# Optimization experiments

Hardware: AMD Instinct MI355X
Metric: run time of the kernel (lower is better)

The kernel has to match this reference:

```python
import jax, jax.numpy as jnp
import numpy as np
import math

V, D, L, FF, H, DH, W, DM, T, B = 32000, 1024, 4, 4096, 16, 64, 256, 64, 1024, 1


def rms_norm(x, w):
    return x * jax.lax.rsqrt(jnp.mean(x * x, axis=-1, keepdims=True) + 1e-6) * w


def setup_inputs() -> dict:
    key = jax.random.key(0)
    ks = jax.random.split(key, 16)
    s = 0.02
    return {
        "x": jax.random.randint(ks[0], (B, T), 0, V),
        "embed": jax.random.normal(ks[1], (V, D), jnp.float32) * s,
        "ln_in_w": jnp.ones((D,), jnp.float32),
        "ln1_w": jnp.ones((L, D), jnp.float32),
        "lnd_w": jnp.ones((L, D), jnp.float32),
        "qkv_w": jax.random.normal(ks[2], (L, 3 * H * DH, D), jnp.float32) * s,
        "swa_out_w": jax.random.normal(ks[3], (L, D, H * DH), jnp.float32) * s,
        "k_w": jax.random.normal(ks[4], (L, H * DM, D), jnp.float32) * s,
        "v_w": jax.random.normal(ks[5], (L, H * DM, D), jnp.float32) * s,
        "q_w": jax.random.normal(ks[6], (L, H * DM, D), jnp.float32) * s,
        "beta_w": jax.random.normal(ks[7], (L, H, D), jnp.float32) * s,
        "mem_out_w": jax.random.normal(ks[8], (L, D, H * DM), jnp.float32) * s,
        "gate_w": jax.random.normal(ks[9], (L, D, D), jnp.float32) * s,
        "comb_w": jax.random.normal(ks[10], (L, D, D), jnp.float32) * s,
        "ln2_w": jnp.ones((L, D), jnp.float32),
        "wg": jax.random.normal(ks[11], (L, FF, D), jnp.float32) * s,
        "wu": jax.random.normal(ks[12], (L, FF, D), jnp.float32) * s,
        "wo": jax.random.normal(ks[13], (L, D, FF), jnp.float32) * s,
        "ln_out_w": jnp.ones((D,), jnp.float32),
    }


def _swa(h1, qkv_w, out_w):
    # h1: [B,T,D]
    qkv = jnp.einsum('btd,ed->bte', h1, qkv_w)  # [B,T,3*H*DH]
    q, k, v = jnp.split(qkv, 3, axis=-1)
    q = q.reshape(h1.shape[0], T, H, DH).transpose(0, 2, 1, 3)
    k = k.reshape(h1.shape[0], T, H, DH).transpose(0, 2, 1, 3)
    v = v.reshape(h1.shape[0], T, H, DH).transpose(0, 2, 1, 3)
    scores = jnp.einsum('bhqd,bhkd->bhqk', q, k) * (DH ** -0.5)
    pos = jnp.arange(T)
    dist = pos[:, None] - pos[None, :]
    allowed = (dist >= 0) & (dist < W)  # causal sliding window
    scores = jnp.where(allowed[None, None], scores, -jnp.inf)
    attn = jax.nn.softmax(scores, axis=-1)
    out = jnp.einsum('bhqk,bhkd->bhqd', attn, v)
    out = out.transpose(0, 2, 1, 3).reshape(h1.shape[0], T, H * DH)
    return jnp.einsum('bte,de->btd', out, out_w)


def _delta(h2, k_w, v_w, q_w, beta_w, mem_out_w):
    Bv = h2.shape[0]
    proj = lambda w: jnp.einsum('btd,ed->bte', h2, w).reshape(Bv, T, H, DM).transpose(0, 2, 1, 3)
    keys, values, queries = proj(k_w), proj(v_w), proj(q_w)
    beta = jax.nn.sigmoid(jnp.einsum('btd,hd->bht', h2, beta_w))  # [B,H,T]
    keys = keys / jnp.maximum(jnp.linalg.norm(keys, axis=-1, keepdims=True), 1e-12)
    queries = queries / jnp.maximum(jnp.linalg.norm(queries, axis=-1, keepdims=True), 1e-12)
    log_retain = jnp.log(1.0 - beta + 1e-8)
    cum_log = jnp.cumsum(log_retain, axis=-1)  # [B,H,T]
    log_decay = cum_log[..., :, None] - cum_log[..., None, :]  # [B,H,T,T]
    causal = jnp.triu(jnp.ones((T, T), dtype=bool))  # matches torch.triu mask in source
    decay = jnp.exp(jnp.minimum(log_decay, 0.0)) * causal
    kq = jnp.einsum('bhid,bhjd->bhij', queries, keys) / math.sqrt(DM)
    weights = kq * decay
    out = jnp.einsum('bhij,bhjd->bhid', weights, values)
    out = out + beta[..., None] * values
    out = out.transpose(0, 2, 1, 3).reshape(Bv, T, H * DM)
    return jnp.einsum('bte,de->btd', out, mem_out_w)


def reference(x, embed, ln_in_w, ln1_w, lnd_w, qkv_w, swa_out_w, k_w, v_w, q_w,
              beta_w, mem_out_w, gate_w, comb_w, ln2_w, wg, wu, wo, ln_out_w):
    h = rms_norm(embed[x], ln_in_w)  # [B,T,D]
    for l in range(L):
        h1 = rms_norm(h, ln1_w[l])
        h2 = rms_norm(h, lnd_w[l])
        local = _swa(h1, qkv_w[l], swa_out_w[l])
        global_ctx = _delta(h2, k_w[l], v_w[l], q_w[l], beta_w[l], mem_out_w[l])
        gate = jax.nn.sigmoid(jnp.einsum('btd,ed->bte', h1, gate_w[l]))
        mixed = jnp.einsum('btd,ed->bte', gate * local + (1.0 - gate) * global_ctx, comb_w[l])
        h = h + mixed
        hn = rms_norm(h, ln2_w[l])
        ffn = jnp.einsum('btf,df->btd', jax.nn.silu(jnp.einsum('btd,fd->btf', hn, wg[l])) * jnp.einsum('btd,fd->btf', hn, wu[l]), wo[l])
        h = h + ffn
    logits = jnp.einsum('btd,vd->btv', rms_norm(h, ln_out_w), embed)  # tied head
    return logits
```

## Files before the change

kernel.cpp:

```cpp
#include <hip/hip_runtime.h>

typedef unsigned short u16;
typedef unsigned int   u32;
typedef __attribute__((ext_vector_type(8))) __bf16 bfv8;
typedef __attribute__((ext_vector_type(4))) float  f32x4;
typedef __attribute__((ext_vector_type(4))) u32    u32x4;

__device__ __forceinline__ u16 f2bf(float f){
  u32 u = __builtin_bit_cast(u32, f);
  return (u16)((u + 0x7FFFu + ((u >> 16) & 1u)) >> 16);
}
__device__ __forceinline__ float bf2f(u16 b){
  return __builtin_bit_cast(float, ((u32)b) << 16);
}
__device__ __forceinline__ u32 pk2(float a, float b){
  return (u32)f2bf(a) | ((u32)f2bf(b) << 16);
}
__device__ __forceinline__ float wsum(float v){
  #pragma unroll
  for (int m = 32; m > 0; m >>= 1) v += __shfl_xor(v, m, 64);
  return v;
}
__device__ __forceinline__ void gload16(const void* g, void* l){
  __builtin_amdgcn_global_load_lds((const __attribute__((address_space(1))) void*)g,
                                   (__attribute__((address_space(3))) void*)l, 16, 0, 0);
}

struct CBatch { const float* s[12]; long long p4[13]; u16* dst; };
__global__ __launch_bounds__(256) void flm_conv(CBatch cb)
{
  const int seg = blockIdx.y;
  const long long base = cb.p4[seg];
  const long long n8 = (cb.p4[seg + 1] - base) >> 1;
  const f32x4* __restrict__ src = (const f32x4*)cb.s[seg];
  u32x4* __restrict__ dst = (u32x4*)cb.dst + (base >> 1);
  for (long long i = (long long)blockIdx.x * 256 + threadIdx.x; i < n8;
       i += (long long)gridDim.x * 256){
    f32x4 v0 = __builtin_nontemporal_load(src + 2*i);
    f32x4 v1 = __builtin_nontemporal_load(src + 2*i + 1);
    u32x4 p;
    p.x = pk2(v0.x, v0.y); p.y = pk2(v0.z, v0.w);
    p.z = pk2(v1.x, v1.y); p.w = pk2(v1.z, v1.w);
    __builtin_nontemporal_store(p, dst + i);
  }
}

struct GDesc {
  const u16* A; const float* Bw; float* Cf; u16* Cb;
  int lda, ldb, ldc, kbeg, kend, blk0, epi, pad;
};
struct GBatch { GDesc d[6]; int ng, total; };

template<bool BW>
__global__ __launch_bounds__(512) void flm_mgemm(GBatch gb)
{
  constexpr int LDK = BW ? 64 : 72;
  __shared__ u16 sA[128][LDK];
  __shared__ u16 sB[128][LDK];
  const int tid = threadIdx.x, lane = tid & 63, w = tid >> 6;

  const int T = gb.total, bid = blockIdx.x;
  const int q8 = T >> 3, r8 = T & 7, xc = bid & 7, of = bid >> 3;
  const int lin = (xc < r8 ? xc * (q8 + 1) : r8 * (q8 + 1) + (xc - r8) * q8) + of;
  int di = 0;
  #pragma unroll
  for (int i = 1; i < 6; i++) if (i < gb.ng && lin >= gb.d[i].blk0) di = i;
  const GDesc g = gb.d[di];
  const int local = lin - g.blk0;
  const int row0 = (local & 7) * 128;
  const int col0 = (local >> 3) * 128;
  const int wr = (w >> 2) * 64, wc = (w & 3) * 32;

  f32x4 acc[4][2];
  #pragma unroll
  for (int m = 0; m < 4; m++)
    #pragma unroll
    for (int n = 0; n < 2; n++)
      acc[m][n] = (f32x4){0.f, 0.f, 0.f, 0.f};

  const int csw = ((lane & 7) ^ (lane >> 3)) * 8;
  const u16* B16 = (const u16*)g.Bw;

  for (int k0 = g.kbeg; k0 < g.kend; k0 += 64){
    if constexpr (BW){
      const u16* a0 = g.A + (size_t)(row0 + w*16 + (lane>>3)) * g.lda + k0 + csw;
      const u16* b0 = B16 + (size_t)(col0 + w*16 + (lane>>3)) * g.ldb + k0 + csw;
      gload16(a0,                     &sA[w*16    ][0]);
      gload16(a0 + (size_t)8*g.lda,   &sA[w*16 + 8][0]);
      gload16(b0,                     &sB[w*16    ][0]);
      gload16(b0 + (size_t)8*g.ldb,   &sB[w*16 + 8][0]);
    } else {
      #pragma unroll
      for (int i = 0; i < 2; i++){
        int idx = tid + i * 512;
        int r = idx >> 3, c = (idx & 7) * 8;
        *(uint4*)&sA[r][c] = *(const uint4*)(g.A + (size_t)(row0 + r) * g.lda + k0 + c);
      }
      #pragma unroll
      for (int i = 0; i < 4; i++){
        int idx = tid + i * 512;
        int r = idx >> 4, c = (idx & 15) * 4;
        float4 v = *(const float4*)(g.Bw + (size_t)(col0 + r) * g.ldb + k0 + c);
        uint2 p; p.x = pk2(v.x, v.y); p.y = pk2(v.z, v.w);
        *(uint2*)&sB[r][c] = p;
      }
    }
    __syncthreads();
    #pragma unroll
    for (int kk = 0; kk < 2; kk++){
      bfv8 af[4], bfr[2];
      #pragma unroll
      for (int m = 0; m < 4; m++){
        int row = wr + m*16 + (lane & 15);
        if constexpr (BW){
          int slot = (kk*4 + (lane >> 4)) ^ (row & 7);
          af[m] = *(const bfv8*)((const char*)sA + row*128 + slot*16);
        } else {
          af[m] = *(const bfv8*)&sA[row][kk*32 + (lane >> 4) * 8];
        }
      }
      #pragma unroll
      for (int n = 0; n < 2; n++){
        int row = wc + n*16 + (lane & 15);
        if constexpr (BW){
          int slot = (kk*4 + (lane >> 4)) ^ (row & 7);
          bfr[n] = *(const bfv8*)((const char*)sB + row*128 + slot*16);
        } else {
          bfr[n] = *(const bfv8*)&sB[row][kk*32 + (lane >> 4) * 8];
        }
      }
      #pragma unroll
      for (int m = 0; m < 4; m++)
        #pragma unroll
        for (int n = 0; n < 2; n++)
          acc[m][n] = __builtin_amdgcn_mfma_f32_16x16x32_bf16(af[m], bfr[n], acc[m][n], 0, 0, 0);
    }
    __syncthreads();
  }

  #pragma unroll
  for (int m = 0; m < 4; m++){
    int rbase = row0 + wr + m*16 + (lane >> 4) * 4;
    #pragma unroll
    for (int n = 0; n < 2; n++){
      int col = col0 + wc + n*16 + (lane & 15);
      if (g.epi == 2){
        uint2 p;
        p.x = pk2(acc[m][n][0], acc[m][n][1]);
        p.y = pk2(acc[m][n][2], acc[m][n][3]);
        *(uint2*)&g.Cb[(size_t)col * g.ldc + rbase] = p;
      } else {
        #pragma unroll
        for (int j = 0; j < 4; j++){
          float v = acc[m][n][j];
          size_t o = (size_t)(rbase + j) * g.ldc + col;
          switch (g.epi){
            case 0: g.Cf[o] = v; break;
            case 1: g.Cb[o] = f2bf(v); break;
            default: atomicAdd(&g.Cf[o], v); break;
          }
        }
      }
    }
  }
}

__global__ __launch_bounds__(256) void flm_mix(
    const float* __restrict__ gr, const float* __restrict__ lo,
    const float* __restrict__ gl, u16* __restrict__ o)
{
  int i = blockIdx.x * 256 + threadIdx.x;
  float4 gv = ((const float4*)gr)[i];
  float4 lv = ((const float4*)lo)[i];
  float4 bv = ((const float4*)gl)[i];
  float sx = 1.f/(1.f+expf(-gv.x)), sy = 1.f/(1.f+expf(-gv.y));
  float sz = 1.f/(1.f+expf(-gv.z)), sw = 1.f/(1.f+expf(-gv.w));
  uint2 p;
  p.x = pk2(sx*lv.x + (1.f-sx)*bv.x, sy*lv.y + (1.f-sy)*bv.y);
  p.y = pk2(sz*lv.z + (1.f-sz)*bv.z, sw*lv.w + (1.f-sw)*bv.w);
  ((uint2*)o)[i] = p;
}

__global__ __launch_bounds__(256) void flm_silu(
    const u16* __restrict__ gg, const u16* __restrict__ uu, u16* __restrict__ o)
{
  int i = blockIdx.x * 256 + threadIdx.x;
  uint2 gv = ((const uint2*)gg)[i];
  uint2 uv = ((const uint2*)uu)[i];
  float g0 = bf2f((u16)gv.x), g1 = bf2f((u16)(gv.x >> 16));
  float g2 = bf2f((u16)gv.y), g3 = bf2f((u16)(gv.y >> 16));
  float u0 = bf2f((u16)uv.x), u1 = bf2f((u16)(uv.x >> 16));
  float u2 = bf2f((u16)uv.y), u3 = bf2f((u16)(uv.y >> 16));
  float a = g0 / (1.f + expf(-g0)) * u0;
  float b = g1 / (1.f + expf(-g1)) * u1;
  float c = g2 / (1.f + expf(-g2)) * u2;
  float d = g3 / (1.f + expf(-g3)) * u3;
  uint2 p; p.x = pk2(a, b); p.y = pk2(c, d);
  ((uint2*)o)[i] = p;
}

__global__ __launch_bounds__(256) void flm_embed(
    const int* __restrict__ x, const float* __restrict__ embed,
    const float* __restrict__ w, float* __restrict__ h)
{
  int t = blockIdx.x, tid = threadIdx.x;
  int tok = x[t];
  float4 v = ((const float4*)(embed + (size_t)tok * 1024))[tid];
  float ss = v.x*v.x + v.y*v.y + v.z*v.z + v.w*v.w;
  ss = wsum(ss);
  __shared__ float red[4];
  if ((tid & 63) == 0) red[tid >> 6] = ss;
  __syncthreads();
  float inv = rsqrtf((red[0]+red[1]+red[2]+red[3]) * (1.f/1024.f) + 1e-6f);
  float4 wv = ((const float4*)w)[tid];
  float4 o; o.x = v.x*inv*wv.x; o.y = v.y*inv*wv.y; o.z = v.z*inv*wv.z; o.w = v.w*inv*wv.w;
  ((float4*)(h + (size_t)t * 1024))[tid] = o;
}

__global__ __launch_bounds__(256) void flm_rms(
    const float* __restrict__ h, const float* __restrict__ w1, const float* __restrict__ w2,
    u16* __restrict__ o1, u16* __restrict__ o2)
{
  int t = blockIdx.x, tid = threadIdx.x;
  float4 v = ((const float4*)(h + (size_t)t * 1024))[tid];
  float ss = v.x*v.x + v.y*v.y + v.z*v.z + v.w*v.w;
  ss = wsum(ss);
  __shared__ float red[4];
  if ((tid & 63) == 0) red[tid >> 6] = ss;
  __syncthreads();
  float inv = rsqrtf((red[0]+red[1]+red[2]+red[3]) * (1.f/1024.f) + 1e-6f);
  {
    float4 wv = ((const float4*)w1)[tid];
    uint2 p; p.x = pk2(v.x*inv*wv.x, v.y*inv*wv.y); p.y = pk2(v.z*inv*wv.z, v.w*inv*wv.w);
    ((uint2*)(o1 + (size_t)t * 1024))[tid] = p;
  }
  if (o2 != nullptr){
    float4 wv = ((const float4*)w2)[tid];
    uint2 p; p.x = pk2(v.x*inv*wv.x, v.y*inv*wv.y); p.y = pk2(v.z*inv*wv.z, v.w*inv*wv.w);
    ((uint2*)(o2 + (size_t)t * 1024))[tid] = p;
  }
}

__global__ __launch_bounds__(64) void flm_betanorm(
    const u16* __restrict__ h2, const float* __restrict__ bw, float* __restrict__ beta,
    u16* __restrict__ keys, u16* __restrict__ queries)
{
  int t = blockIdx.x, lane = threadIdx.x;
  float hv[16];
  #pragma unroll
  for (int i = 0; i < 16; i++) hv[i] = bf2f(h2[(size_t)t*1024 + i*64 + lane]);
  for (int h = 0; h < 16; h++){
    float p = 0.f;
    #pragma unroll
    for (int i = 0; i < 16; i++) p += hv[i] * bw[h*1024 + i*64 + lane];
    p = wsum(p);
    if (lane == 0) beta[t*16 + h] = 1.f / (1.f + expf(-p));
  }
  #pragma unroll
  for (int h = 0; h < 16; h++){
    size_t idx = (size_t)t * 1024 + h * 64 + lane;
    float v = bf2f(keys[idx]);
    float nrm = fmaxf(sqrtf(wsum(v * v)), 1e-12f);
    keys[idx] = f2bf(v / nrm);
    float q = bf2f(queries[idx]);
    float qn = fmaxf(sqrtf(wsum(q * q)), 1e-12f);
    queries[idx] = f2bf(q / qn);
  }
}

__global__ __launch_bounds__(256) void flm_attn(
    const u16* __restrict__ qkvb, const u16* __restrict__ qvT,
    const u16* __restrict__ keys, const u16* __restrict__ valT, const u16* __restrict__ queries,
    const float* __restrict__ beta, u16* __restrict__ aout, u16* __restrict__ dout)
{
  __shared__ u16 sK[64][72];
  __shared__ u16 sVt[64][72];
  __shared__ u16 sP[4][16][72];
  const int tid = threadIdx.x, lane = tid & 63, w = tid >> 6;
  const int qt = blockIdx.x, h = blockIdx.y;
  const int base = h * 64;
  const int ri = w*16 + (lane>>4)*4;

  if (blockIdx.z == 0){
    bfv8 aq[2];
    {
      int qrow = qt*64 + w*16 + (lane & 15);
      #pragma unroll
      for (int kk = 0; kk < 2; kk++)
        aq[kk] = *(const bfv8*)(qkvb + (size_t)qrow*2048 + base + kk*32 + (lane>>4)*8);
    }
    f32x4 acc_o[4];
    float m_r[4], l_r[4];
    #pragma unroll
    for (int n = 0; n < 4; n++) acc_o[n] = (f32x4){0.f,0.f,0.f,0.f};
    #pragma unroll
    for (int r = 0; r < 4; r++){ m_r[r] = -1e30f; l_r[r] = 0.f; }
    const int jt0 = (qt >= 4) ? qt - 4 : 0;

    for (int jt = qt; jt >= jt0; jt--){
      #pragma unroll
      for (int i = 0; i < 2; i++){
        int idx = tid + i*256;
        int r = idx >> 3, c = (idx & 7) * 8;
        *(uint4*)&sK[r][c] = *(const uint4*)(qkvb + (size_t)(jt*64+r)*2048 + 1024 + base + c);
        *(uint4*)&sVt[r][c] = *(const uint4*)(qvT + (size_t)(base + r)*1024 + jt*64 + c);
      }
      __syncthreads();

      f32x4 sv[4];
      #pragma unroll
      for (int n = 0; n < 4; n++) sv[n] = (f32x4){0.f,0.f,0.f,0.f};
      #pragma unroll
      for (int kk = 0; kk < 2; kk++){
        #pragma unroll
        for (int n = 0; n < 4; n++){
          bfv8 bk = *(const bfv8*)&sK[n*16 + (lane & 15)][(lane>>4)*8 + kk*32];
          sv[n] = __builtin_amdgcn_mfma_f32_16x16x32_bf16(aq[kk], bk, sv[n], 0, 0, 0);
        }
      }
      #pragma unroll
      for (int n = 0; n < 4; n++){
        int cj = n*16 + (lane & 15);
        #pragma unroll
        for (int r = 0; r < 4; r++){
          float s = sv[n][r] * 0.125f;
          if (jt == qt)      { if (cj > ri + r) s = -1e30f; }
          else if (jt == jt0 && qt - jt0 == 4) { if (cj <= ri + r) s = -1e30f; }
          sv[n][r] = s;
        }
      }
      float pv[4][4], scl[4];
      #pragma unroll
      for (int r = 0; r < 4; r++){
        float mx = -1e30f;
        #pragma unroll
        for (int n = 0; n < 4; n++) mx = fmaxf(mx, sv[n][r]);
        #pragma unroll
        for (int m = 1; m < 16; m <<= 1) mx = fmaxf(mx, __shfl_xor(mx, m, 64));
        float mn = fmaxf(m_r[r], mx);
        float sc = expf(m_r[r] - mn);
        m_r[r] = mn; scl[r] = sc;
        float rs = 0.f;
        #pragma unroll
        for (int n = 0; n < 4; n++){ float p = expf(sv[n][r] - mn); pv[n][r] = p; rs += p; }
        #pragma unroll
        for (int m = 1; m < 16; m <<= 1) rs += __shfl_xor(rs, m, 64);
        l_r[r] = l_r[r] * sc + rs;
      }
      #pragma unroll
      for (int n = 0; n < 4; n++){
        #pragma unroll
        for (int r = 0; r < 4; r++){
          acc_o[n][r] *= scl[r];
          sP[w][(lane>>4)*4 + r][n*16 + (lane & 15)] = f2bf(pv[n][r]);
        }
      }
      #pragma unroll
      for (int kk = 0; kk < 2; kk++){
        bfv8 ap = *(const bfv8*)&sP[w][lane & 15][(lane>>4)*8 + kk*32];
        #pragma unroll
        for (int n = 0; n < 4; n++){
          bfv8 bv = *(const bfv8*)&sVt[n*16 + (lane & 15)][(lane>>4)*8 + kk*32];
          acc_o[n] = __builtin_amdgcn_mfma_f32_16x16x32_bf16(ap, bv, acc_o[n], 0, 0, 0);
        }
      }
      __syncthreads();
    }

    #pragma unroll
    for (int n = 0; n < 4; n++){
      int col = base + n*16 + (lane & 15);
      #pragma unroll
      for (int r = 0; r < 4; r++){
        int row = qt*64 + ri + r;
        aout[(size_t)row*1024 + col] = f2bf(acc_o[n][r] / l_r[r]);
      }
    }
  } else {
    bfv8 aq[2];
    {
      int qrow = qt*64 + w*16 + (lane & 15);
      #pragma unroll
      for (int kk = 0; kk < 2; kk++)
        aq[kk] = *(const bfv8*)(queries + (size_t)qrow*1024 + base + kk*32 + (lane>>4)*8);
    }
    f32x4 acc_o[4];
    #pragma unroll
    for (int n = 0; n < 4; n++) acc_o[n] = (f32x4){0.f,0.f,0.f,0.f};

    for (int jt = qt; jt < 16; jt++){
      #pragma unroll
      for (int i = 0; i < 2; i++){
        int idx = tid + i*256;
        int r = idx >> 3, c = (idx & 7) * 8;
        *(uint4*)&sK[r][c] = *(const uint4*)(keys + (size_t)(jt*64+r)*1024 + base + c);
        *(uint4*)&sVt[r][c] = *(const uint4*)(valT + (size_t)(base + r)*1024 + jt*64 + c);
      }
      __syncthreads();

      f32x4 sv[4];
      #pragma unroll
      for (int n = 0; n < 4; n++) sv[n] = (f32x4){0.f,0.f,0.f,0.f};
      #pragma unroll
      for (int kk = 0; kk < 2; kk++){
        #pragma unroll
        for (int n = 0; n < 4; n++){
          bfv8 bk = *(const bfv8*)&sK[n*16 + (lane & 15)][(lane>>4)*8 + kk*32];
          sv[n] = __builtin_amdgcn_mfma_f32_16x16x32_bf16(aq[kk], bk, sv[n], 0, 0, 0);
        }
      }
      #pragma unroll
      for (int n = 0; n < 4; n++){
        int cj = n*16 + (lane & 15);
        #pragma unroll
        for (int r = 0; r < 4; r++){
          float p = sv[n][r] * 0.125f;
          if (jt == qt && cj < ri + r) p = 0.f;
          sP[w][(lane>>4)*4 + r][n*16 + (lane & 15)] = f2bf(p);
        }
      }
      #pragma unroll
      for (int kk = 0; kk < 2; kk++){
        bfv8 ap = *(const bfv8*)&sP[w][lane & 15][(lane>>4)*8 + kk*32];
        #pragma unroll
        for (int n = 0; n < 4; n++){
          bfv8 bv = *(const bfv8*)&sVt[n*16 + (lane & 15)][(lane>>4)*8 + kk*32];
          acc_o[n] = __builtin_amdgcn_mfma_f32_16x16x32_bf16(ap, bv, acc_o[n], 0, 0, 0);
        }
      }
      __syncthreads();
    }

    #pragma unroll
    for (int n = 0; n < 4; n++){
      int col = base + n*16 + (lane & 15);
      #pragma unroll
      for (int r = 0; r < 4; r++){
        int row = qt*64 + ri + r;
        float b = beta[row*16 + h];
        float v = bf2f(valT[(size_t)col*1024 + row]);
        dout[(size_t)row*1024 + col] = f2bf(acc_o[n][r] + b * v);
      }
    }
  }
}

static GDesc mkd(const u16* A, int lda, const float* Bw, int ldb,
                 float* Cf, u16* Cb, int ldc,
                 int kbeg, int kend, int blk0, int epi){
  GDesc d; d.A=A; d.Bw=Bw; d.Cf=Cf; d.Cb=Cb;
  d.lda=lda; d.ldb=ldb; d.ldc=ldc; d.kbeg=kbeg; d.kend=kend; d.blk0=blk0; d.epi=epi; d.pad=0;
  return d;
}

extern "C" void kernel_launch(void* const* d_in, const int* in_sizes, int n_in,
                              void* d_out, int out_size, void* d_ws, size_t ws_size,
                              hipStream_t stream)
{
  (void)in_sizes; (void)n_in; (void)out_size;
  const int*   x        = (const int*)d_in[0];
  const float* embed    = (const float*)d_in[1];
  const float* ln_in_w  = (const float*)d_in[2];
  const float* ln1_w    = (const float*)d_in[3];
  const float* lnd_w    = (const float*)d_in[4];
  const float* qkv_w    = (const float*)d_in[5];
  const float* swa_out_w= (const float*)d_in[6];
  const float* k_w      = (const float*)d_in[7];
  const float* v_w      = (const float*)d_in[8];
  const float* q_w      = (const float*)d_in[9];
  const float* beta_w   = (const float*)d_in[10];
  const float* mem_out_w= (const float*)d_in[11];
  const float* gate_w   = (const float*)d_in[12];
  const float* comb_w   = (const float*)d_in[13];
  const float* ln2_w    = (const float*)d_in[14];
  const float* wg       = (const float*)d_in[15];
  const float* wu       = (const float*)d_in[16];
  const float* wo       = (const float*)d_in[17];
  const float* ln_out_w = (const float*)d_in[18];
  float* out = (float*)d_out;

  char* ws = (char*)d_ws;
  const size_t KB = 1024, MB = 1u << 20;
  float* h       = (float*)(ws + 0);
  u16*   h1      = (u16*)  (ws + 4*MB);
  u16*   h2      = (u16*)  (ws + 6*MB);
  u16*   qkvb    = (u16*)  (ws + 8*MB);
  u16*   qvT     = (u16*)  (ws + 12*MB);
  u16*   keys    = (u16*)  (ws + 14*MB);
  u16*   valT    = (u16*)  (ws + 16*MB);
  u16*   queries = (u16*)  (ws + 18*MB);
  float* beta    = (float*)(ws + 20*MB);
  u16*   attn    = (u16*)  (ws + 20*MB + 256*KB);
  u16*   delt    = (u16*)  (ws + 22*MB + 256*KB);
  float* lo0     = (float*)(ws + 24*MB + 256*KB);
  float* gl0     = (float*)(ws + 28*MB + 256*KB);
  float* gbuf    = (float*)(ws + 32*MB + 256*KB);
  u16*   mcomb   = (u16*)  (ws + 36*MB + 256*KB);
  u16*   hn      = (u16*)  (ws + 38*MB + 256*KB);
  u16*   g16     = (u16*)  (ws + 4*MB);
  u16*   u16b    = (u16*)  (ws + 12*MB);
  u16*   sbuf    = (u16*)  (ws + 20*MB);

  u16* wb = (u16*)(ws + 41*MB);
  size_t off = 0; auto nx = [&](size_t n){ size_t o = off; off += n; return o; };
  const size_t nEmb = 32768000ULL, nQkv = 12582912ULL, nSq = 4194304ULL, nFf = 16777216ULL;
  u16* wemb  = wb + nx(nEmb);
  u16* wqkv  = wb + nx(nQkv);
  u16* wswa  = wb + nx(nSq);
  u16* wk    = wb + nx(nSq);
  u16* wv    = wb + nx(nSq);
  u16* wq    = wb + nx(nSq);
  u16* wmem  = wb + nx(nSq);
  u16* wgate = wb + nx(nSq);
  u16* wcomb = wb + nx(nSq);
  u16* wwg   = wb + nx(nFf);
  u16* wwu   = wb + nx(nFf);
  u16* wwo   = wb + nx(nFf);
  const size_t NEED = 41*MB + off * 2;
  const bool bw = (ws_size >= NEED);

  auto MG = [&](int nblk, GBatch& gbv){
    if (bw) flm_mgemm<true><<<nblk, 512, 0, stream>>>(gbv);
    else    flm_mgemm<false><<<nblk, 512, 0, stream>>>(gbv);
  };

  if (bw){
    CBatch cb;
    const float* srcs[12] = {embed, qkv_w, swa_out_w, k_w, v_w, q_w,
                             mem_out_w, gate_w, comb_w, wg, wu, wo};
    const size_t ns[12] = {nEmb, nQkv, nSq, nSq, nSq, nSq, nSq, nSq, nSq, nFf, nFf, nFf};
    long long acc4 = 0;
    for (int i = 0; i < 12; i++){ cb.s[i] = srcs[i]; cb.p4[i] = acc4; acc4 += (long long)(ns[i] >> 2); }
    cb.p4[12] = acc4; cb.dst = wb;
    flm_conv<<<dim3(1024, 12), 256, 0, stream>>>(cb);
  }

  flm_embed<<<1024, 256, 0, stream>>>(x, embed, ln_in_w, h);

  for (int l = 0; l < 4; l++){
    const size_t lq = (size_t)l * 3145728, ls = (size_t)l * 1048576, lf = (size_t)l * 4194304;
    const float* Wqkv  = bw ? (const float*)(wqkv  + lq) : qkv_w     + lq;
    const float* WqkvV = bw ? (const float*)(wqkv  + lq + 2048*1024ULL) : qkv_w + lq + 2048*1024ULL;
    const float* Wk    = bw ? (const float*)(wk    + ls) : k_w       + ls;
    const float* Wv    = bw ? (const float*)(wv    + ls) : v_w       + ls;
    const float* Wq    = bw ? (const float*)(wq    + ls) : q_w       + ls;
    const float* Wswa  = bw ? (const float*)(wswa  + ls) : swa_out_w + ls;
    const float* Wmem  = bw ? (const float*)(wmem  + ls) : mem_out_w + ls;
    const float* Wgate = bw ? (const float*)(wgate + ls) : gate_w    + ls;
    const float* Wcomb = bw ? (const float*)(wcomb + ls) : comb_w    + ls;
    const float* Wwg   = bw ? (const float*)(wwg   + lf) : wg        + lf;
    const float* Wwu   = bw ? (const float*)(wwu   + lf) : wu        + lf;
    const float* Wwo   = bw ? (const float*)(wwo   + lf) : wo        + lf;

    flm_rms<<<1024, 256, 0, stream>>>(h, ln1_w + l*1024, lnd_w + l*1024, h1, h2);

    {
      GBatch gb;
      gb.d[0] = mkd(h1, 1024, Wqkv,  1024, nullptr, qkvb,    2048, 0, 1024, 0,   1);
      gb.d[1] = mkd(h1, 1024, WqkvV, 1024, nullptr, qvT,     1024, 0, 1024, 128, 2);
      gb.d[2] = mkd(h2, 1024, Wk,    1024, nullptr, keys,    1024, 0, 1024, 192, 1);
      gb.d[3] = mkd(h2, 1024, Wv,    1024, nullptr, valT,    1024, 0, 1024, 256, 2);
      gb.d[4] = mkd(h2, 1024, Wq,    1024, nullptr, queries, 1024, 0, 1024, 320, 1);
      gb.d[5] = mkd(h1, 1024, Wgate, 1024, gbuf,    nullptr, 1024, 0, 1024, 384, 0);
      gb.ng = 6; gb.total = 448;
      MG(448, gb);
    }
    flm_betanorm<<<1024, 64, 0, stream>>>(h2, beta_w + (size_t)l*16*1024, beta, keys, queries);
    flm_attn<<<dim3(16, 16, 2), 256, 0, stream>>>(qkvb, qvT, keys, valT, queries, beta, attn, delt);

    {
      GBatch gb;
      gb.d[0] = mkd(attn, 1024, Wswa, 1024, lo0, nullptr, 1024, 0, 1024, 0, 0);
      gb.d[1] = mkd(delt, 1024, Wmem, 1024, gl0, nullptr, 1024, 0, 1024, 64, 0);
      gb.d[2] = gb.d[1]; gb.d[2].blk0 = 0x7fffffff;
      gb.d[3] = gb.d[2]; gb.d[4] = gb.d[2]; gb.d[5] = gb.d[2];
      gb.ng = 2; gb.total = 128;
      MG(128, gb);
    }
    flm_mix<<<1024, 256, 0, stream>>>(gbuf, lo0, gl0, mcomb);
    {
      GBatch gb;
      gb.d[0] = mkd(mcomb, 1024, Wcomb, 1024, h, nullptr, 1024, 0, 512, 0, 5);
      gb.d[1] = mkd(mcomb, 1024, Wcomb, 1024, h, nullptr, 1024, 512, 1024, 64, 5);
      gb.d[2] = gb.d[1]; gb.d[2].blk0 = 0x7fffffff;
      gb.d[3] = gb.d[2]; gb.d[4] = gb.d[2]; gb.d[5] = gb.d[2];
      gb.ng = 2; gb.total = 128;
      MG(128, gb);
    }
    flm_rms<<<1024, 256, 0, stream>>>(h, ln2_w + l*1024, nullptr, hn, nullptr);
    {
      GBatch gb;
      gb.d[0] = mkd(hn, 1024, Wwg, 1024, nullptr, g16, 4096, 0, 1024, 0, 1);
      gb.d[1] = mkd(hn, 1024, Wwu, 1024, nullptr, u16b, 4096, 0, 1024, 256, 1);
      gb.d[2] = gb.d[1]; gb.d[2].blk0 = 0x7fffffff;
      gb.d[3] = gb.d[2]; gb.d[4] = gb.d[2]; gb.d[5] = gb.d[2];
      gb.ng = 2; gb.total = 512;
      MG(512, gb);
    }
    flm_silu<<<4096, 256, 0, stream>>>(g16, u16b, sbuf);
    {
      GBatch gb;
      for (int s = 0; s < 4; s++)
        gb.d[s] = mkd(sbuf, 4096, Wwo, 4096, h, nullptr, 1024, s*1024, (s+1)*1024, s*64, 5);
      gb.d[4] = gb.d[3]; gb.d[4].blk0 = 0x7fffffff;
      gb.d[5] = gb.d[4];
      gb.ng = 4; gb.total = 256;
      MG(256, gb);
    }
  }

  flm_rms<<<1024, 256, 0, stream>>>(h, ln_out_w, nullptr, hn, nullptr);
  {
    GBatch gb;
    gb.d[0] = mkd(hn, 1024, bw ? (const float*)wemb : embed, 1024, out, nullptr, 32000,
                  0, 1024, 0, 0);
    gb.d[1] = gb.d[0]; gb.d[1].blk0 = 0x7fffffff;
    gb.d[2] = gb.d[1]; gb.d[3] = gb.d[1]; gb.d[4] = gb.d[1]; gb.d[5] = gb.d[1];
    gb.ng = 1; gb.total = 2000;
    MG(2000, gb);
  }
}
```

Baseline: 1.001 ms.

## Split-K the attention output projections and fold partial sums into the mix kernel

The SWA-output and memory-output GEMMs each split their K dimension into two halves, doubling the block count from 128 to 256 so more CUs are busy. Each half writes to its own fp32 buffer, and a new mix kernel adds the two partials before applying the gate. This costs extra workspace and extra fp32 traffic in the mix step. Separately, float-to-bf16 conversion now uses the native __bf16 cast instead of manual bit rounding.

```diff
diff --git a/kernel.cpp b/kernel.cpp
--- a/kernel.cpp
+++ b/kernel.cpp
@@ -7,8 +7,8 @@
 typedef __attribute__((ext_vector_type(4))) u32    u32x4;
 
 __device__ __forceinline__ u16 f2bf(float f){
-  u32 u = __builtin_bit_cast(u32, f);
-  return (u16)((u + 0x7FFFu + ((u >> 16) & 1u)) >> 16);
+  __bf16 b = (__bf16)f;
+  return __builtin_bit_cast(u16, b);
 }
 __device__ __forceinline__ float bf2f(u16 b){
   return __builtin_bit_cast(float, ((u32)b) << 16);
@@ -163,6 +163,24 @@
       }
     }
   }
+}
+
+__global__ __launch_bounds__(256) void flm_mix5(
+    const float* __restrict__ gr, const float* __restrict__ lo0, const float* __restrict__ lo1,
+    const float* __restrict__ gl0, const float* __restrict__ gl1, u16* __restrict__ o)
+{
+  int i = blockIdx.x * 256 + threadIdx.x;
+  float4 gv = ((const float4*)gr)[i];
+  float4 l0 = ((const float4*)lo0)[i];
+  float4 l1 = ((const float4*)lo1)[i];
+  float4 b0 = ((const float4*)gl0)[i];
+  float4 b1 = ((const float4*)gl1)[i];
+  float sx = 1.f/(1.f+expf(-gv.x)), sy = 1.f/(1.f+expf(-gv.y));
+  float sz = 1.f/(1.f+expf(-gv.z)), sw = 1.f/(1.f+expf(-gv.w));
+  uint2 p;
+  p.x = pk2(sx*(l0.x+l1.x) + (1.f-sx)*(b0.x+b1.x), sy*(l0.y+l1.y) + (1.f-sy)*(b0.y+b1.y));
+  p.y = pk2(sz*(l0.z+l1.z) + (1.f-sz)*(b0.z+b1.z), sw*(l0.w+l1.w) + (1.f-sw)*(b0.w+b1.w));
+  ((uint2*)o)[i] = p;
 }
 
 __global__ __launch_bounds__(256) void flm_mix(
@@ -493,15 +511,17 @@
   u16*   attn    = (u16*)  (ws + 20*MB + 256*KB);
   u16*   delt    = (u16*)  (ws + 22*MB + 256*KB);
   float* lo0     = (float*)(ws + 24*MB + 256*KB);
-  float* gl0     = (float*)(ws + 28*MB + 256*KB);
-  float* gbuf    = (float*)(ws + 32*MB + 256*KB);
-  u16*   mcomb   = (u16*)  (ws + 36*MB + 256*KB);
-  u16*   hn      = (u16*)  (ws + 38*MB + 256*KB);
+  float* lo1     = (float*)(ws + 28*MB + 256*KB);
+  float* gl0     = (float*)(ws + 32*MB + 256*KB);
+  float* gl1     = (float*)(ws + 36*MB + 256*KB);
+  float* gbuf    = (float*)(ws + 40*MB + 256*KB);
+  u16*   mcomb   = (u16*)  (ws + 44*MB + 256*KB);
+  u16*   hn      = (u16*)  (ws + 46*MB + 256*KB);
   u16*   g16     = (u16*)  (ws + 4*MB);
   u16*   u16b    = (u16*)  (ws + 12*MB);
   u16*   sbuf    = (u16*)  (ws + 20*MB);
 
-  u16* wb = (u16*)(ws + 41*MB);
+  u16* wb = (u16*)(ws + 48*MB + 512*KB);
   size_t off = 0; auto nx = [&](size_t n){ size_t o = off; off += n; return o; };
   const size_t nEmb = 32768000ULL, nQkv = 12582912ULL, nSq = 4194304ULL, nFf = 16777216ULL;
   u16* wemb  = wb + nx(nEmb);
@@ -516,7 +536,7 @@
   u16* wwg   = wb + nx(nFf);
   u16* wwu   = wb + nx(nFf);
   u16* wwo   = wb + nx(nFf);
-  const size_t NEED = 41*MB + off * 2;
+  const size_t NEED = 48*MB + 512*KB + off * 2;
   const bool bw = (ws_size >= NEED);
 
   auto MG = [&](int nblk, GBatch& gbv){
@@ -568,7 +588,18 @@
     flm_betanorm<<<1024, 64, 0, stream>>>(h2, beta_w + (size_t)l*16*1024, beta, keys, queries);
     flm_attn<<<dim3(16, 16, 2), 256, 0, stream>>>(qkvb, qvT, keys, valT, queries, beta, attn, delt);
 
-    {
+    if (bw){
+      GBatch gb;
+      gb.d[0] = mkd(attn, 1024, Wswa, 1024, lo0, nullptr, 1024, 0,   512,  0,   0);
+      gb.d[1] = mkd(attn, 1024, Wswa, 1024, lo1, nullptr, 1024, 512, 1024, 64,  0);
+      gb.d[2] = mkd(delt, 1024, Wmem, 1024, gl0, nullptr, 1024, 0,   512,  128, 0);
+      gb.d[3] = mkd(delt, 1024, Wmem, 1024, gl1, nullptr, 1024, 512, 1024, 192, 0);
+      gb.d[4] = gb.d[3]; gb.d[4].blk0 = 0x7fffffff;
+      gb.d[5] = gb.d[4];
+      gb.ng = 4; gb.total = 256;
+      MG(256, gb);
+      flm_mix5<<<1024, 256, 0, stream>>>(gbuf, lo0, lo1, gl0, gl1, mcomb);
+    } else {
       GBatch gb;
       gb.d[0] = mkd(attn, 1024, Wswa, 1024, lo0, nullptr, 1024, 0, 1024, 0, 0);
       gb.d[1] = mkd(delt, 1024, Wmem, 1024, gl0, nullptr, 1024, 0, 1024, 64, 0);
@@ -576,8 +607,9 @@
       gb.d[3] = gb.d[2]; gb.d[4] = gb.d[2]; gb.d[5] = gb.d[2];
       gb.ng = 2; gb.total = 128;
       MG(128, gb);
-    }
-    flm_mix<<<1024, 256, 0, stream>>>(gbuf, lo0, gl0, mcomb);
+      flm_mix<<<1024, 256, 0, stream>>>(gbuf, lo0, gl0, mcomb);
+    }
+
     {
       GBatch gb;
       gb.d[0] = mkd(mcomb, 1024, Wcomb, 1024, h, nullptr, 1024, 0, 512, 0, 5);
```

Measured after the change: 971.5 us. 3.0% less time.
